# Kernel tuning notes

Measured on AMD Instinct MI355X. Metric: run time of the kernel, lower is better.

Reference implementation:

```python
import jax, jax.numpy as jnp
import numpy as np

WS = 7            # cubic window
HEADS = 6
DIM = 96          # attention channel dim (concat of two half-streams)
CH = 48           # per-stream channels (dim // 2)
HID = 384         # int(dim * mlp_ratio)
N = WS ** 3       # 343 tokens per window
EPS = 1e-5


def _rel_pos_index():
    c = np.stack(np.meshgrid(np.arange(WS), np.arange(WS), np.arange(WS), indexing='ij')).reshape(3, -1)
    rel = (c[:, :, None] - c[:, None, :]).transpose(1, 2, 0) + (WS - 1)
    rel[:, :, 0] *= (2 * WS - 1) * (2 * WS - 1)
    rel[:, :, 1] *= (2 * WS - 1)
    return rel.sum(-1)  # (N, N) int

RPI = jnp.asarray(_rel_pos_index())


def _ln(x, g, b):
    m = x.mean(-1, keepdims=True)
    v = ((x - m) ** 2).mean(-1, keepdims=True)
    return (x - m) * jax.lax.rsqrt(v + EPS) * g + b


def _win_part(x):
    B, H, W, T, C = x.shape
    x = x.reshape(B, H // WS, WS, W // WS, WS, T // WS, WS, C)
    return x.transpose(0, 1, 3, 5, 2, 4, 6, 7).reshape(-1, WS, WS, WS, C)


def _win_rev(w, B, H, W, T):
    C = w.shape[-1]
    x = w.reshape(B, H // WS, W // WS, T // WS, WS, WS, WS, C)
    return x.transpose(0, 1, 4, 2, 5, 3, 6, 7).reshape(B, H, W, T, C)


def _chessboard(wa, wb, gd, gh, gw):
    C = wa.shape[-1]
    a = wa.reshape(gd, gh, gw, WS, WS, WS, C)
    b = wb.reshape(gd, gh, gw, WS, WS, WS, C)
    i = jnp.arange(gd)[:, None, None]
    j = jnp.arange(gh)[None, :, None]
    k = jnp.arange(gw)[None, None, :]
    m = (((i + j + k) % 2) == 0)[..., None, None, None, None]
    return (jnp.where(m, a, b).reshape(-1, WS, WS, WS, C),
            jnp.where(m, b, a).reshape(-1, WS, WS, WS, C))


def _attn(x, mask, rpb, qkv_w, qkv_b, proj_w, proj_b):
    B_, n, C = x.shape
    hd = C // HEADS
    qkv = (x @ qkv_w + qkv_b).reshape(B_, n, 3, HEADS, hd).transpose(2, 0, 3, 1, 4)
    q, k, v = qkv[0] * (hd ** -0.5), qkv[1], qkv[2]
    att = jnp.einsum('bhnd,bhmd->bhnm', q, k)
    att = att + rpb[RPI].transpose(2, 0, 1)[None]   # relative position bias gather
    att = att + mask[:, None]                        # shift mask; B_ == nW since B == 1
    att = jax.nn.softmax(att, axis=-1)
    out = jnp.einsum('bhnm,bhmd->bhnd', att, v).transpose(0, 2, 1, 3).reshape(B_, n, C)
    return out @ proj_w + proj_b


def _mlp(x, w1, b1, w2, b2):
    return jax.nn.gelu(x @ w1 + b1, approximate=False) @ w2 + b2


def _forward(x_a, x_b, mask_matrix, n1a_g, n1a_b, n1b_g, n1b_b,
             rpb_a, qkvw_a, qkvb_a, projw_a, projb_a,
             rpb_b, qkvw_b, qkvb_b, projw_b, projb_b,
             n2a_g, n2a_b, n2b_g, n2b_b,
             fc1w_a, fc1b_a, fc2w_a, fc2b_a, fc1w_b, fc1b_b, fc2w_b, fc2b_b,
             gw1, gw2, gb2, H, W, T):
    B, L, _ = x_a.shape
    sa0, sb0 = x_a, x_b
    a = _ln(x_a, n1a_g, n1a_b).reshape(B, H, W, T, CH)
    b = _ln(x_b, n1b_g, n1b_b).reshape(B, H, W, T, CH)
    # chessboard cross-stream shuffle of windows (shifted-window branch)
    ca, cb = _chessboard(_win_part(a), _win_part(b), H // WS, W // WS, T // WS)
    a_cr = _win_rev(ca, B, H, W, T)
    b_cr = _win_rev(cb, B, H, W, T)
    neg, pos, dims = (-3, -3, -3), (3, 3, 3), (1, 2, 3)
    sa, sb = jnp.roll(a, neg, dims), jnp.roll(b, neg, dims)
    sac, sbc = jnp.roll(a_cr, neg, dims), jnp.roll(b_cr, neg, dims)
    xa_w = _win_part(jnp.concatenate([sa, sbc], -1)).reshape(-1, N, DIM)
    xb_w = _win_part(jnp.concatenate([sb, sac], -1)).reshape(-1, N, DIM)
    oa = _attn(xa_w, mask_matrix, rpb_a, qkvw_a, qkvb_a, projw_a, projb_a)
    ob = _attn(xb_w, mask_matrix, rpb_b, qkvw_b, qkvb_b, projw_b, projb_b)
    oa = jnp.roll(_win_rev(oa.reshape(-1, WS, WS, WS, DIM), B, H, W, T), pos, dims)[..., :CH].reshape(B, L, CH)
    ob = jnp.roll(_win_rev(ob.reshape(-1, WS, WS, WS, DIM), B, H, W, T), pos, dims)[..., :CH].reshape(B, L, CH)
    x_a = sa0 + oa
    x_b = sb0 + ob
    x_a = x_a + _mlp(_ln(x_a, n2a_g, n2a_b), fc1w_a, fc1b_a, fc2w_a, fc2b_a)
    x_b = x_b + _mlp(_ln(x_b, n2b_g, n2b_b), fc1w_b, fc1b_b, fc2w_b, fc2b_b)
    g = jax.nn.sigmoid(jnp.maximum(x_a.mean(1) @ gw1, 0.0) @ gw2 + gb2)[:, :, None]  # (B,1,1)
    x_a = x_a + g * x_b
    return x_a, x_b


def setup_inputs():
    key = jax.random.key(0)
    ks = iter(jax.random.split(key, 24))
    H = W = T = 35
    L = H * W * T
    nW = (H // WS) * (W // WS) * (T // WS)
    p = lambda shape: jax.random.normal(next(ks), shape, jnp.float32) * 0.02
    d = {
        'x_a': jax.random.normal(next(ks), (1, L, CH), jnp.float32),
        'x_b': jax.random.normal(next(ks), (1, L, CH), jnp.float32),
        'mask_matrix': jax.random.normal(next(ks), (nW, N, N), jnp.float32),
        'n1a_g': jnp.ones((CH,), jnp.float32), 'n1a_b': jnp.zeros((CH,), jnp.float32),
        'n1b_g': jnp.ones((CH,), jnp.float32), 'n1b_b': jnp.zeros((CH,), jnp.float32),
        'rpb_a': p(((2 * WS - 1) ** 3, HEADS)),
        'qkvw_a': p((DIM, 3 * DIM)), 'qkvb_a': jnp.zeros((3 * DIM,), jnp.float32),
        'projw_a': p((DIM, DIM)), 'projb_a': jnp.zeros((DIM,), jnp.float32),
        'rpb_b': p(((2 * WS - 1) ** 3, HEADS)),
        'qkvw_b': p((DIM, 3 * DIM)), 'qkvb_b': jnp.zeros((3 * DIM,), jnp.float32),
        'projw_b': p((DIM, DIM)), 'projb_b': jnp.zeros((DIM,), jnp.float32),
        'n2a_g': jnp.ones((CH,), jnp.float32), 'n2a_b': jnp.zeros((CH,), jnp.float32),
        'n2b_g': jnp.ones((CH,), jnp.float32), 'n2b_b': jnp.zeros((CH,), jnp.float32),
        'fc1w_a': p((CH, HID)), 'fc1b_a': jnp.zeros((HID,), jnp.float32),
        'fc2w_a': p((HID, CH)), 'fc2b_a': jnp.zeros((CH,), jnp.float32),
        'fc1w_b': p((CH, HID)), 'fc1b_b': jnp.zeros((HID,), jnp.float32),
        'fc2w_b': p((HID, CH)), 'fc2b_b': jnp.zeros((CH,), jnp.float32),
        'gw1': p((CH, CH // 4)), 'gw2': p((CH // 4, 1)),
        'gb2': jnp.full((1,), -2.0, jnp.float32),
        'H': H, 'W': W, 'T': T,
    }
    return d


def reference(x_a, x_b, mask_matrix, n1a_g, n1a_b, n1b_g, n1b_b,
              rpb_a, qkvw_a, qkvb_a, projw_a, projb_a,
              rpb_b, qkvw_b, qkvb_b, projw_b, projb_b,
              n2a_g, n2a_b, n2b_g, n2b_b,
              fc1w_a, fc1b_a, fc2w_a, fc2b_a, fc1w_b, fc1b_b, fc2w_b, fc2b_b,
              gw1, gw2, gb2, H, W, T):
    return _forward(x_a, x_b, mask_matrix, n1a_g, n1a_b, n1b_g, n1b_b,
                    rpb_a, qkvw_a, qkvb_a, projw_a, projb_a,
                    rpb_b, qkvw_b, qkvb_b, projw_b, projb_b,
                    n2a_g, n2a_b, n2b_g, n2b_b,
                    fc1w_a, fc1b_a, fc2w_a, fc2b_a, fc1w_b, fc1b_b, fc2w_b, fc2b_b,
                    gw1, gw2, gb2, H, W, T)
```

## Files before the change

kernel.cpp:

```cpp
#include <hip/hip_runtime.h>
#include <hip/hip_fp16.h>

#define LQ    42875
#define NTOK  343
#define X1SZ  2058000

#define OFF_MEAN 0
#define OFF_QKV  36928
#define OFF_WF   12500000
#define OFF_RPB  12600000
#define OFF_MASKH 13400000
#define QKV_BYTES_NEEDED 56100000ull
#define MASKH_BYTES_NEEDED 83100000ull

typedef _Float16 f16x8 __attribute__((ext_vector_type(8)));
typedef float f32x4 __attribute__((ext_vector_type(4)));
union B128 { uint4 u; f16x8 h; _Float16 e[8]; };
union U2H { unsigned u; __half2 h; };

__device__ __forceinline__ int src_index(int w, int i, int& par) {
  int gi = w / 25, gj = (w / 5) % 5, gk = w % 5;
  int ph = i / 49, pw = (i / 7) % 7, pt = i % 7;
  int hs = gi * 7 + ph + 3; if (hs >= 35) hs -= 35;
  int wd = gj * 7 + pw + 3; if (wd >= 35) wd -= 35;
  int td = gk * 7 + pt + 3; if (td >= 35) td -= 35;
  par = ((hs / 7) + (wd / 7) + (td / 7)) & 1;
  return (hs * 35 + wd) * 35 + td;
}

__global__ __launch_bounds__(64) void k_init(float* __restrict__ ws) {
  if (threadIdx.x < 49) ws[threadIdx.x] = 0.f;
}

__global__ __launch_bounds__(256) void k_pack(
    const float* __restrict__ w1a, const float* __restrict__ w1b,
    const float* __restrict__ w2a, const float* __restrict__ w2b,
    const float* __restrict__ qwa, const float* __restrict__ qwb,
    float* __restrict__ ws) {
  int idx = blockIdx.x * 256 + threadIdx.x;
  if (idx >= 17664) return;
  uint4* WFB = (uint4*)(ws + OFF_WF);
  unsigned short h[8];
  uint4* dst;
  if (idx < 10752) {
    int s = idx / 5376, r = idx - s * 5376;
    uint4* WF = WFB + (size_t)s * 5376;
    if (r < 3072) {
      int jn = r / 128, t = r - jn * 128, kk = t / 64, lane = t - kk * 64;
      int q = lane >> 4, n = lane & 15;
      const float* w1 = s ? w1b : w1a;
      int j = jn * 16 + n;
#pragma unroll
      for (int e = 0; e < 8; e++) {
        int k = kk * 32 + q * 8 + e;
        float v = (k < 48) ? w1[k * 384 + j] : 0.f;
        h[e] = __half_as_ushort(__float2half(v));
      }
    } else {
      int rr = r - 3072;
      int kt = rr / 192, t = rr - kt * 192, cn = t / 64, lane = t - cn * 64;
      int q = lane >> 4, n = lane & 15;
      const float* w2 = s ? w2b : w2a;
      int c = cn * 16 + n;
#pragma unroll
      for (int e = 0; e < 8; e++) {
        int j = kt * 32 + q * 8 + e;
        h[e] = __half_as_ushort(__float2half(w2[j * 48 + c]));
      }
    }
    dst = WF + r;
  } else {
    int idx2 = idx - 10752;
    int s = idx2 / 3456, r = idx2 - s * 3456;
    int jn = r / 192, t = r - jn * 192, kk = t / 64, lane = t - kk * 64;
    int q = lane >> 4, n = lane & 15;
    const float* qw = s ? qwb : qwa;
    int j = jn * 16 + n;
#pragma unroll
    for (int e = 0; e < 8; e++) {
      int k = kk * 32 + q * 8 + e;
      h[e] = __half_as_ushort(__float2half(qw[k * 288 + j]));
    }
    dst = WFB + 10752 + (size_t)s * 3456 + r;
  }
  uint4 u;
  u.x = (unsigned)h[0] | ((unsigned)h[1] << 16);
  u.y = (unsigned)h[2] | ((unsigned)h[3] << 16);
  u.z = (unsigned)h[4] | ((unsigned)h[5] << 16);
  u.w = (unsigned)h[6] | ((unsigned)h[7] << 16);
  *dst = u;
}

__global__ __launch_bounds__(256) void k_rpb(
    const float* __restrict__ rpa, const float* __restrict__ rpbp,
    float* __restrict__ ws) {
  int sh = blockIdx.y;
  int s = sh / 6, h = sh - s * 6;
  int idx = blockIdx.x * 256 + threadIdx.x;
  if (idx >= 117649) return;
  int ir = idx / 343, j = idx - ir * 343;
  int bi = (ir / 49) * 169 + ((ir / 7) % 7) * 13 + (ir % 7) + 1098;
  int bj = (j / 49) * 169 + ((j / 7) % 7) * 13 + (j % 7);
  const float* rp = s ? rpbp : rpa;
  ((__half*)(ws + OFF_RPB))[(size_t)sh * 117992 + ir * 344 + j] =
      __float2half(rp[(bi - bj) * 6 + h]);
}

__global__ __launch_bounds__(256) void k_maskh(
    const float* __restrict__ mask, __half* __restrict__ mh) {
  int row = blockIdx.x;
  const float* src = mask + (size_t)row * 343;
  __half* dst = mh + (size_t)row * 344;
  for (int c = threadIdx.x; c < 343; c += 256)
    dst[c] = __float2half(src[c]);
  if (threadIdx.x == 0) dst[343] = __float2half(0.f);
}

__global__ __launch_bounds__(256) void k_qkv(
    const float* __restrict__ xa, const float* __restrict__ xb,
    const float* __restrict__ ga, const float* __restrict__ ba,
    const float* __restrict__ gb, const float* __restrict__ bb,
    const float* __restrict__ qba, const float* __restrict__ qbb,
    const float* __restrict__ ws, __half* __restrict__ qkvh) {
  __shared__ uint4 LDSB[2368];
  int s = blockIdx.z;
  int tid = threadIdx.x;
  int wid = tid >> 6, lane = tid & 63;
  int quad = lane >> 4, n15 = lane & 15;
  uint4* WR = LDSB + wid * 592;
  _Float16* th = (_Float16*)WR;
  int tbase = blockIdx.x * 64 + wid * 16;

  if (lane < 32) {
    int tt = lane & 15, which = lane >> 4;
    int t = tbase + tt;
    float v[48];
    bool wr = false, dup = false;
    if (t < LQ) {
      int w = t / 343, i = t - w * 343;
      int par; int src = src_index(w, i, par);
      const float* xr; const float* G; const float* B;
      bool doit;
      if (which == 0) { xr = (s ? xb : xa) + src * 48; G = s ? gb : ga; B = s ? bb : ba; doit = true; dup = (par == 1); }
      else            { xr = (s ? xa : xb) + src * 48; G = s ? ga : gb; B = s ? ba : bb; doit = (par == 0); }
      if (doit) {
        float sm = 0.f, sq = 0.f;
#pragma unroll
        for (int q4 = 0; q4 < 12; q4++) {
          float4 tv = ((const float4*)xr)[q4];
          v[4 * q4] = tv.x; v[4 * q4 + 1] = tv.y; v[4 * q4 + 2] = tv.z; v[4 * q4 + 3] = tv.w;
          sm += tv.x + tv.y + tv.z + tv.w;
          sq += tv.x * tv.x + tv.y * tv.y + tv.z * tv.z + tv.w * tv.w;
        }
        float m = sm * (1.f / 48.f);
        float r = rsqrtf(sq * (1.f / 48.f) - m * m + 1e-5f);
#pragma unroll
        for (int k = 0; k < 48; k++) v[k] = (v[k] - m) * r * G[k] + B[k];
        wr = true;
      }
    } else if (which == 0) {
#pragma unroll
      for (int k = 0; k < 48; k++) v[k] = 0.f;
      wr = true; dup = true;
    }
    if (wr) {
#pragma unroll
      for (int c6 = 0; c6 < 6; c6++) {
        unsigned short h[8];
#pragma unroll
        for (int e = 0; e < 8; e++) h[e] = __half_as_ushort(__float2half(v[c6 * 8 + e]));
        uint4 u;
        u.x = (unsigned)h[0] | ((unsigned)h[1] << 16);
        u.y = (unsigned)h[2] | ((unsigned)h[3] << 16);
        u.z = (unsigned)h[4] | ((unsigned)h[5] << 16);
        u.w = (unsigned)h[6] | ((unsigned)h[7] << 16);
        WR[(which * 6 + c6) * 16 + tt] = u;
        if (dup) WR[(6 + c6) * 16 + tt] = u;
      }
    }
  }

  B128 ax0, ax1, ax2;
  ax0.u = WR[(0 + quad) * 16 + n15];
  ax1.u = WR[(4 + quad) * 16 + n15];
  ax2.u = WR[(8 + quad) * 16 + n15];

  const uint4* QF = (const uint4*)(ws + OFF_WF) + 10752 + (size_t)s * 3456;
  const float* QB = s ? qbb : qba;
  const f32x4 ZC = {0.f, 0.f, 0.f, 0.f};

  for (int jn = 0; jn < 18; jn++) {
    B128 b0, b1, b2;
    b0.u = QF[(jn * 3 + 0) * 64 + lane];
    b1.u = QF[(jn * 3 + 1) * 64 + lane];
    b2.u = QF[(jn * 3 + 2) * 64 + lane];
    f32x4 c = __builtin_amdgcn_mfma_f32_16x16x32_f16(ax0.h, b0.h, ZC, 0, 0, 0);
    c = __builtin_amdgcn_mfma_f32_16x16x32_f16(ax1.h, b1.h, c, 0, 0, 0);
    c = __builtin_amdgcn_mfma_f32_16x16x32_f16(ax2.h, b2.h, c, 0, 0, 0);
    float bias = QB[jn * 16 + n15];
    float scale = (jn < 6) ? 0.25f : 1.0f;
#pragma unroll
    for (int r = 0; r < 4; r++)
      th[(quad * 4 + r) * 296 + jn * 16 + n15] = (_Float16)((c[r] + bias) * scale);
  }
  for (int e = lane; e < 576; e += 64) {
    int row = e / 36, cc = e - row * 36;
    int t = tbase + row;
    if (t < LQ)
      ((uint4*)qkvh)[(size_t)(s * LQ + t) * 36 + cc] = WR[row * 37 + cc];
  }
}

template <bool H16>
__global__ __launch_bounds__(256) void k_attn(
    const __half* __restrict__ rpbmat,
    const void* __restrict__ maskp, __half* __restrict__ qkvh) {
  int bid = blockIdx.x;
  int xcd = bid & 7, q8 = bid >> 3;
  int u = q8 / 12, inst = q8 - u * 12;
  int w = u * 8 + xcd;
  if (w >= 125) return;
  int s = inst & 1, h = inst >> 1;

  __shared__ uint4 FRAG[1664];
  uint4* Kf4 = FRAG;
  uint4* Vf4 = FRAG + 704;
  _Float16* Vfh = (_Float16*)(FRAG + 704);
  _Float16* Pbh = (_Float16*)(FRAG + 1408);

  int tid = threadIdx.x;
  const uint4 Z4 = {0u, 0u, 0u, 0u};
  for (int e = tid; e < 1408; e += 256) FRAG[e] = Z4;
  __syncthreads();

  size_t wbase = (size_t)((s * 125 + w) * NTOK) * 288;
  for (int i = tid; i < NTOK; i += 256) {
    const uint4* row = (const uint4*)(qkvh + wbase + (size_t)i * 288) + (h * 2);
    uint4 k0 = row[12], k1 = row[13];
    B128 v0, v1; v0.u = row[24]; v1.u = row[25];
    int n = i & 15, it = i >> 4;
    Kf4[it * 32 + n] = k0;
    Kf4[it * 32 + 16 + n] = k1;
    int vbase = ((i >> 5) * 64 + ((i >> 3) & 3) * 16) * 8 + (i & 7);
#pragma unroll
    for (int d = 0; d < 8; d++) {
      Vfh[vbase + d * 8] = v0.e[d];
      Vfh[vbase + (d + 8) * 8] = v1.e[d];
    }
  }
  __syncthreads();

  int wid = tid >> 6, lane = tid & 63;
  int quad = lane >> 4, n15 = lane & 15;
  const f32x4 ZC = {0.f, 0.f, 0.f, 0.f};
  __half* obh = qkvh;
  const __half* rbase = rpbmat + (size_t)(s * 6 + h) * 117992;

  _Float16* Pw = Pbh + wid * 512;
  int slotA = quad ^ (n15 & 6);
  int slotB = (4 + quad) ^ (n15 & 6);
  int rslot = (2 * quad) ^ (n15 & 6);
  int ja0 = quad * 4;

  for (int it = wid; it < 22; it += 4) {
    int i0 = it * 16;
    int irow = i0 + n15; if (irow > 342) irow = 342;
    const __half* rrow = rbase + (size_t)irow * 344;
    const __half* mrow = nullptr; const float* mrowf = nullptr;
    if constexpr (H16) mrow = (const __half*)maskp + ((size_t)w * 343 + irow) * 344;
    else mrowf = (const float*)maskp + ((size_t)w * 343 + irow) * 343;

    B128 qbits;
    int qtok = i0 + n15;
    if (quad < 2 && qtok < NTOK)
      qbits.u = *((const uint4*)(qkvh + wbase + (size_t)qtok * 288) + h * 2 + (quad & 1));
    else
      qbits.u = Z4;
    f32x4 acc = ZC;
    float ls = 0.f;

    float bcur[8], bnxt[8];
    auto loadb = [&](int jt, float* b) {
      if constexpr (H16) {
        const __half* mp = mrow + jt * 32 + ja0;
        const __half* rp2 = rrow + jt * 32 + ja0;
        uint2 ma = *(const uint2*)mp;
        uint2 mb = *(const uint2*)(mp + 16);
        uint2 ra = *(const uint2*)rp2;
        uint2 rb = *(const uint2*)(rp2 + 16);
        U2H x0, x1, x2, x3, y0, y1, y2, y3;
        x0.u = ma.x; x1.u = ma.y; x2.u = mb.x; x3.u = mb.y;
        y0.u = ra.x; y1.u = ra.y; y2.u = rb.x; y3.u = rb.y;
        float2 f;
        f = __half22float2(__hadd2(x0.h, y0.h)); b[0] = f.x; b[1] = f.y;
        f = __half22float2(__hadd2(x1.h, y1.h)); b[2] = f.x; b[3] = f.y;
        f = __half22float2(__hadd2(x2.h, y2.h)); b[4] = f.x; b[5] = f.y;
        f = __half22float2(__hadd2(x3.h, y3.h)); b[6] = f.x; b[7] = f.y;
      } else {
        const float* mp = mrowf + jt * 32 + ja0;
        const __half* rp2 = rrow + jt * 32 + ja0;
#pragma unroll
        for (int r = 0; r < 4; r++) {
          b[r] = mp[r] + __half2float(rp2[r]);
          b[4 + r] = mp[16 + r] + __half2float(rp2[16 + r]);
        }
      }
    };
    loadb(0, bcur);

    for (int j32 = 0; j32 < 11; j32++) {
      if (j32 < 10) loadb(j32 + 1, bnxt);
      B128 kb0, kb1;
      kb0.u = Kf4[(j32 * 2) * 32 + ((quad & 1) << 4) + n15];
      kb1.u = Kf4[(j32 * 2 + 1) * 32 + ((quad & 1) << 4) + n15];
      if (quad >= 2) { kb0.u = Z4; kb1.u = Z4; }
      f32x4 s0 = __builtin_amdgcn_mfma_f32_16x16x32_f16(kb0.h, qbits.h, ZC, 0, 0, 0);
      f32x4 s1 = __builtin_amdgcn_mfma_f32_16x16x32_f16(kb1.h, qbits.h, ZC, 0, 0, 0);
      bool last = (j32 == 10);
      float p0[4], p1[4];
#pragma unroll
      for (int r = 0; r < 4; r++) {
        float b1 = bcur[4 + r];
        if (last && (quad * 4 + r) >= 7) b1 = -1e30f;
        p0[r] = __expf(s0[r] + bcur[r]);
        p1[r] = __expf(s1[r] + b1);
        ls += p0[r] + p1[r];
      }
      U2H c0, c1, c2, c3;
      c0.h = __floats2half2_rn(p0[0], p0[1]);
      c1.h = __floats2half2_rn(p0[2], p0[3]);
      c2.h = __floats2half2_rn(p1[0], p1[1]);
      c3.h = __floats2half2_rn(p1[2], p1[3]);
      uint2 w0; w0.x = c0.u; w0.y = c1.u;
      uint2 w1; w1.x = c2.u; w1.y = c3.u;
      *(uint2*)(Pw + n15 * 32 + slotA * 4) = w0;
      *(uint2*)(Pw + n15 * 32 + slotB * 4) = w1;
      B128 pa, vbits;
      pa.u = *(const uint4*)(Pw + n15 * 32 + rslot * 4);
      vbits.u = Vf4[j32 * 64 + lane];
      acc = __builtin_amdgcn_mfma_f32_16x16x32_f16(pa.h, vbits.h, acc, 0, 0, 0);
#pragma unroll
      for (int e = 0; e < 8; e++) bcur[e] = bnxt[e];
    }
    ls += __shfl_xor(ls, 16);
    ls += __shfl_xor(ls, 32);
#pragma unroll
    for (int r = 0; r < 4; r++) {
      float lr = __shfl(ls, quad * 4 + r);
      int ir = i0 + quad * 4 + r;
      if (ir < 343)
        obh[wbase + (size_t)ir * 288 + h * 16 + n15] = __float2half(acc[r] * (1.f / lr));
    }
  }
}

__global__ __launch_bounds__(384) void k_proj(
    const __half* __restrict__ qkvh,
    const float* __restrict__ xa0, const float* __restrict__ xb0,
    const float* __restrict__ pwa, const float* __restrict__ pba,
    const float* __restrict__ pwb, const float* __restrict__ pbb,
    float* __restrict__ out) {
  int sw = blockIdx.x; int s = sw / 125, w = sw - s * 125;
  int i = threadIdx.x;
  if (i >= NTOK) return;
  const float* Wt = s ? pwb : pwa;
  const float* Bi = s ? pbb : pba;
  const uint4* orow = (const uint4*)(qkvh + (size_t)((s * 125 + w) * NTOK + i) * 288);
  float acc[48];
#pragma unroll
  for (int c = 0; c < 48; c++) acc[c] = 0.f;
#pragma unroll
  for (int k8 = 0; k8 < 12; k8++) {
    B128 ov; ov.u = orow[k8];
#pragma unroll
    for (int e = 0; e < 8; e++) {
      float x = (float)ov.e[e];
      const float* wr = Wt + (k8 * 8 + e) * 96;
#pragma unroll
      for (int c = 0; c < 48; c++) acc[c] = fmaf(x, wr[c], acc[c]);
    }
  }
  int par; int src = src_index(w, i, par);
  const float* x0 = (s ? xb0 : xa0) + src * 48;
  float* dst = out + s * X1SZ + src * 48;
#pragma unroll
  for (int q = 0; q < 12; q++) {
    float4 xv = ((const float4*)x0)[q];
    float4 o;
    o.x = xv.x + acc[4 * q + 0] + Bi[4 * q + 0];
    o.y = xv.y + acc[4 * q + 1] + Bi[4 * q + 1];
    o.z = xv.z + acc[4 * q + 2] + Bi[4 * q + 2];
    o.w = xv.w + acc[4 * q + 3] + Bi[4 * q + 3];
    ((float4*)dst)[q] = o;
  }
}

__global__ __launch_bounds__(256) void k_mlp(
    const float* __restrict__ g2a, const float* __restrict__ b2a,
    const float* __restrict__ g2b, const float* __restrict__ b2b,
    const float* __restrict__ fb1a, const float* __restrict__ fb2a,
    const float* __restrict__ fb1b, const float* __restrict__ fb2b,
    float* __restrict__ out, float* __restrict__ ws) {
  __shared__ uint4 Xf[512];
  __shared__ uint4 tbu[320];
  __shared__ float red[48];
  int s = blockIdx.z;
  int tid = threadIdx.x;
  int wid = tid >> 6, lane = tid & 63;
  int quad = lane >> 4, n15 = lane & 15;
  if (tid < 48) red[tid] = 0.f;
  __syncthreads();

  const float* B1 = s ? fb1b : fb1a;
  const float* B2 = s ? fb2b : fb2a;
  const uint4* W1F = (const uint4*)(ws + OFF_WF) + (size_t)s * 5376;
  const uint4* W2F = W1F + 3072;
  int tbase = blockIdx.x * 64 + wid * 16;
  float* outs = out + (size_t)s * X1SZ;

  if (lane < 16) {
    int t = tbase + lane;
    float v[48];
    if (t < LQ) {
      const float* row = outs + (size_t)t * 48;
      float sm = 0.f, sq = 0.f;
#pragma unroll
      for (int q4 = 0; q4 < 12; q4++) {
        float4 tv = ((const float4*)row)[q4];
        v[4 * q4] = tv.x; v[4 * q4 + 1] = tv.y; v[4 * q4 + 2] = tv.z; v[4 * q4 + 3] = tv.w;
        sm += tv.x + tv.y + tv.z + tv.w;
        sq += tv.x * tv.x + tv.y * tv.y + tv.z * tv.z + tv.w * tv.w;
      }
      float m = sm * (1.f / 48.f);
      float r = rsqrtf(sq * (1.f / 48.f) - m * m + 1e-5f);
      const float* G = s ? g2b : g2a;
      const float* B = s ? b2b : b2a;
#pragma unroll
      for (int k = 0; k < 48; k++) v[k] = (v[k] - m) * r * G[k] + B[k];
    } else {
#pragma unroll
      for (int k = 0; k < 48; k++) v[k] = 0.f;
    }
#pragma unroll
    for (int kc = 0; kc < 8; kc++) {
      uint4 u = {0u, 0u, 0u, 0u};
      if (kc < 6) {
        unsigned short h[8];
#pragma unroll
        for (int e = 0; e < 8; e++) h[e] = __half_as_ushort(__float2half(v[kc * 8 + e]));
        u.x = (unsigned)h[0] | ((unsigned)h[1] << 16);
        u.y = (unsigned)h[2] | ((unsigned)h[3] << 16);
        u.z = (unsigned)h[4] | ((unsigned)h[5] << 16);
        u.w = (unsigned)h[6] | ((unsigned)h[7] << 16);
      }
      Xf[wid * 128 + kc * 16 + lane] = u;
    }
  }

  _Float16* mytb = (_Float16*)(tbu + wid * 80);
  const uint4* mytb4 = tbu + wid * 80;
  const f32x4 ZC = {0.f, 0.f, 0.f, 0.f};
  f32x4 oacc[3] = {ZC, ZC, ZC};
  B128 ax0, ax1;
  ax0.u = Xf[wid * 128 + quad * 16 + n15];
  ax1.u = Xf[wid * 128 + (4 + quad) * 16 + n15];

  for (int kt = 0; kt < 12; kt++) {
    int jn0 = kt * 2, jn1 = jn0 + 1;
    B128 w0, w1, w2, w3;
    w0.u = W1F[jn0 * 128 + lane];
    w1.u = W1F[jn0 * 128 + 64 + lane];
    w2.u = W1F[jn1 * 128 + lane];
    w3.u = W1F[jn1 * 128 + 64 + lane];
    f32x4 a0 = __builtin_amdgcn_mfma_f32_16x16x32_f16(ax0.h, w0.h, ZC, 0, 0, 0);
    a0 = __builtin_amdgcn_mfma_f32_16x16x32_f16(ax1.h, w1.h, a0, 0, 0, 0);
    f32x4 a1 = __builtin_amdgcn_mfma_f32_16x16x32_f16(ax0.h, w2.h, ZC, 0, 0, 0);
    a1 = __builtin_amdgcn_mfma_f32_16x16x32_f16(ax1.h, w3.h, a1, 0, 0, 0);
    float bz0 = B1[jn0 * 16 + n15], bz1 = B1[jn1 * 16 + n15];
#pragma unroll
    for (int r = 0; r < 4; r++) {
      float h0 = a0[r] + bz0;
      h0 = 0.5f * h0 * (1.f + erff(h0 * 0.70710678118654752f));
      float h1 = a1[r] + bz1;
      h1 = 0.5f * h1 * (1.f + erff(h1 * 0.70710678118654752f));
      int rowb = (quad * 4 + r) * 40;
      mytb[rowb + n15] = (_Float16)h0;
      mytb[rowb + 16 + n15] = (_Float16)h1;
    }
    B128 pa; pa.u = mytb4[n15 * 5 + quad];
    B128 c0, c1, c2;
    c0.u = W2F[kt * 192 + lane];
    c1.u = W2F[kt * 192 + 64 + lane];
    c2.u = W2F[kt * 192 + 128 + lane];
    oacc[0] = __builtin_amdgcn_mfma_f32_16x16x32_f16(pa.h, c0.h, oacc[0], 0, 0, 0);
    oacc[1] = __builtin_amdgcn_mfma_f32_16x16x32_f16(pa.h, c1.h, oacc[1], 0, 0, 0);
    oacc[2] = __builtin_amdgcn_mfma_f32_16x16x32_f16(pa.h, c2.h, oacc[2], 0, 0, 0);
  }

  float b2v[3];
#pragma unroll
  for (int cn = 0; cn < 3; cn++) b2v[cn] = B2[cn * 16 + n15];
  float gsum[3] = {0.f, 0.f, 0.f};
#pragma unroll
  for (int r = 0; r < 4; r++) {
    int t = tbase + quad * 4 + r;
    bool val = t < LQ;
    float* orow = outs + (size_t)(val ? t : 0) * 48;
#pragma unroll
    for (int cn = 0; cn < 3; cn++) {
      float fin = 0.f;
      if (val) {
        fin = orow[cn * 16 + n15] + oacc[cn][r] + b2v[cn];
        orow[cn * 16 + n15] = fin;
      }
      gsum[cn] += fin;
    }
  }
  if (s == 0) {
#pragma unroll
    for (int cn = 0; cn < 3; cn++) {
      float v = gsum[cn];
      v += __shfl_xor(v, 16); v += __shfl_xor(v, 32);
      if (quad == 0) atomicAdd(&red[cn * 16 + n15], v);
    }
  }
  __syncthreads();
  if (s == 0 && tid < 48) atomicAdd(ws + OFF_MEAN + tid, red[tid]);
}

__global__ __launch_bounds__(64) void k_gate(
    const float* __restrict__ ws_mean, const float* __restrict__ gw1,
    const float* __restrict__ gw2, const float* __restrict__ gb2,
    float* __restrict__ g) {
  int j = threadIdx.x;
  float t = 0.f;
  if (j < 12) {
    for (int c = 0; c < 48; c++)
      t = fmaf(ws_mean[c] * (1.f / (float)LQ), gw1[c * 12 + j], t);
    t = fmaxf(t, 0.f) * gw2[j];
  }
  for (int off = 32; off > 0; off >>= 1) t += __shfl_down(t, off);
  if (j == 0) *g = 1.f / (1.f + __expf(-(t + gb2[0])));
}

__global__ __launch_bounds__(256) void k_gadd(float* __restrict__ out,
                                              const float* __restrict__ g) {
  int i = blockIdx.x * 256 + threadIdx.x;
  if (i >= X1SZ / 4) return;
  float gv = *g;
  float4* a = (float4*)out;
  const float4* b = (const float4*)(out + X1SZ);
  float4 x = a[i], y = b[i];
  x.x = fmaf(gv, y.x, x.x);
  x.y = fmaf(gv, y.y, x.y);
  x.z = fmaf(gv, y.z, x.z);
  x.w = fmaf(gv, y.w, x.w);
  a[i] = x;
}

extern "C" void kernel_launch(void* const* d_in, const int* in_sizes, int n_in,
                              void* d_out, int out_size, void* d_ws, size_t ws_size,
                              hipStream_t stream) {
  const float* xa    = (const float*)d_in[0];
  const float* xb    = (const float*)d_in[1];
  const float* mask  = (const float*)d_in[2];
  const float* n1ag  = (const float*)d_in[3];
  const float* n1ab  = (const float*)d_in[4];
  const float* n1bg  = (const float*)d_in[5];
  const float* n1bb  = (const float*)d_in[6];
  const float* rpba  = (const float*)d_in[7];
  const float* qkvwa = (const float*)d_in[8];
  const float* qkvba = (const float*)d_in[9];
  const float* pwa   = (const float*)d_in[10];
  const float* pba   = (const float*)d_in[11];
  const float* rpbb  = (const float*)d_in[12];
  const float* qkvwb = (const float*)d_in[13];
  const float* qkvbb = (const float*)d_in[14];
  const float* pwb   = (const float*)d_in[15];
  const float* pbb   = (const float*)d_in[16];
  const float* n2ag  = (const float*)d_in[17];
  const float* n2ab  = (const float*)d_in[18];
  const float* n2bg  = (const float*)d_in[19];
  const float* n2bb  = (const float*)d_in[20];
  const float* w1a   = (const float*)d_in[21];
  const float* fb1a  = (const float*)d_in[22];
  const float* w2a   = (const float*)d_in[23];
  const float* fb2a  = (const float*)d_in[24];
  const float* w1b   = (const float*)d_in[25];
  const float* fb1b  = (const float*)d_in[26];
  const float* w2b   = (const float*)d_in[27];
  const float* fb2b  = (const float*)d_in[28];
  const float* gw1   = (const float*)d_in[29];
  const float* gw2   = (const float*)d_in[30];
  const float* gb2   = (const float*)d_in[31];
  float* ws  = (float*)d_ws;
  float* out = (float*)d_out;

  if (ws_size < QKV_BYTES_NEEDED) return;
  __half* qkvh = (__half*)(ws + OFF_QKV);
  bool bigmask = ws_size >= MASKH_BYTES_NEEDED;

  hipLaunchKernelGGL(k_init, dim3(1), dim3(64), 0, stream, ws);
  hipLaunchKernelGGL(k_pack, dim3(69), dim3(256), 0, stream,
                     w1a, w1b, w2a, w2b, qkvwa, qkvwb, ws);
  hipLaunchKernelGGL(k_rpb, dim3(460, 12), dim3(256), 0, stream,
                     rpba, rpbb, ws);
  if (bigmask)
    hipLaunchKernelGGL(k_maskh, dim3(42875), dim3(256), 0, stream,
                       mask, (__half*)(ws + OFF_MASKH));
  hipLaunchKernelGGL(k_qkv, dim3(670, 1, 2), dim3(256), 0, stream,
                     xa, xb, n1ag, n1ab, n1bg, n1bb,
                     qkvba, qkvbb, ws, qkvh);
  if (bigmask)
    hipLaunchKernelGGL((k_attn<true>), dim3(1536), dim3(256), 0, stream,
                       (const __half*)(ws + OFF_RPB),
                       (const void*)(ws + OFF_MASKH), qkvh);
  else
    hipLaunchKernelGGL((k_attn<false>), dim3(1536), dim3(256), 0, stream,
                       (const __half*)(ws + OFF_RPB), (const void*)mask, qkvh);
  hipLaunchKernelGGL(k_proj, dim3(250), dim3(384), 0, stream,
                     qkvh, xa, xb, pwa, pba, pwb, pbb, out);
  hipLaunchKernelGGL(k_mlp, dim3(670, 1, 2), dim3(256), 0, stream,
                     n2ag, n2ab, n2bg, n2bb,
                     fb1a, fb2a, fb1b, fb2b, out, ws);
  hipLaunchKernelGGL(k_gate, dim3(1), dim3(64), 0, stream,
                     ws + OFF_MEAN, gw1, gw2, gb2, ws + OFF_MEAN + 48);
  hipLaunchKernelGGL(k_gadd, dim3(2011), dim3(256), 0, stream,
                     out, ws + OFF_MEAN + 48);
}
```

Measured before the change: 449.1 us.

## Feed softmax probabilities to PV MFMA from registers, fuse small kernels

Reorders the V fragment layout in LDS so that the attention probabilities computed by each lane can be passed straight from registers as the A operand of the PV MFMA. This removes the per-tile LDS write, read and transpose of P and shrinks shared memory. The gate computation is folded into the gated-add kernel, each block recomputing the scalar gate, and the accumulator zeroing is merged into the pack kernel, which removes two launches. The mask fp16 conversion is vectorised to four elements per thread.

```diff
diff --git a/kernel.cpp b/kernel.cpp
--- a/kernel.cpp
+++ b/kernel.cpp
@@ -28,15 +28,12 @@
   return (hs * 35 + wd) * 35 + td;
 }
 
-__global__ __launch_bounds__(64) void k_init(float* __restrict__ ws) {
-  if (threadIdx.x < 49) ws[threadIdx.x] = 0.f;
-}
-
 __global__ __launch_bounds__(256) void k_pack(
     const float* __restrict__ w1a, const float* __restrict__ w1b,
     const float* __restrict__ w2a, const float* __restrict__ w2b,
     const float* __restrict__ qwa, const float* __restrict__ qwb,
     float* __restrict__ ws) {
+  if (blockIdx.x == 0 && threadIdx.x < 49) ws[OFF_MEAN + threadIdx.x] = 0.f;
   int idx = blockIdx.x * 256 + threadIdx.x;
   if (idx >= 17664) return;
   uint4* WFB = (uint4*)(ws + OFF_WF);
@@ -108,12 +105,19 @@
 
 __global__ __launch_bounds__(256) void k_maskh(
     const float* __restrict__ mask, __half* __restrict__ mh) {
-  int row = blockIdx.x;
-  const float* src = mask + (size_t)row * 343;
-  __half* dst = mh + (size_t)row * 344;
-  for (int c = threadIdx.x; c < 343; c += 256)
-    dst[c] = __float2half(src[c]);
-  if (threadIdx.x == 0) dst[343] = __float2half(0.f);
+  int idx = blockIdx.x * 256 + threadIdx.x;
+  if (idx >= 42875 * 86) return;
+  int row = idx / 86, c = (idx - row * 86) * 4;
+  const float* src = mask + (size_t)row * 343 + c;
+  float v0 = src[0];
+  float v1 = (c + 1 < 343) ? src[1] : 0.f;
+  float v2 = (c + 2 < 343) ? src[2] : 0.f;
+  float v3 = (c + 3 < 343) ? src[3] : 0.f;
+  U2H a, b;
+  a.h = __floats2half2_rn(v0, v1);
+  b.h = __floats2half2_rn(v2, v3);
+  uint2 o; o.x = a.u; o.y = b.u;
+  *(uint2*)(mh + (size_t)row * 344 + c) = o;
 }
 
 __global__ __launch_bounds__(256) void k_qkv(
@@ -222,11 +226,10 @@
   if (w >= 125) return;
   int s = inst & 1, h = inst >> 1;
 
-  __shared__ uint4 FRAG[1664];
+  __shared__ uint4 FRAG[1408];
   uint4* Kf4 = FRAG;
   uint4* Vf4 = FRAG + 704;
   _Float16* Vfh = (_Float16*)(FRAG + 704);
-  _Float16* Pbh = (_Float16*)(FRAG + 1408);
 
   int tid = threadIdx.x;
   const uint4 Z4 = {0u, 0u, 0u, 0u};
@@ -241,11 +244,15 @@
     int n = i & 15, it = i >> 4;
     Kf4[it * 32 + n] = k0;
     Kf4[it * 32 + 16 + n] = k1;
-    int vbase = ((i >> 5) * 64 + ((i >> 3) & 3) * 16) * 8 + (i & 7);
+    int il = i & 31, t5 = i >> 5;
+    int qq, ee;
+    if (il < 16) { qq = il >> 2; ee = il & 3; }
+    else { qq = (il - 16) >> 2; ee = 4 + ((il - 16) & 3); }
+    int vb = (t5 * 64 + qq * 16) * 8 + ee;
 #pragma unroll
     for (int d = 0; d < 8; d++) {
-      Vfh[vbase + d * 8] = v0.e[d];
-      Vfh[vbase + (d + 8) * 8] = v1.e[d];
+      Vfh[vb + d * 8] = v0.e[d];
+      Vfh[vb + (d + 8) * 8] = v1.e[d];
     }
   }
   __syncthreads();
@@ -255,11 +262,6 @@
   const f32x4 ZC = {0.f, 0.f, 0.f, 0.f};
   __half* obh = qkvh;
   const __half* rbase = rpbmat + (size_t)(s * 6 + h) * 117992;
-
-  _Float16* Pw = Pbh + wid * 512;
-  int slotA = quad ^ (n15 & 6);
-  int slotB = (4 + quad) ^ (n15 & 6);
-  int rslot = (2 * quad) ^ (n15 & 6);
   int ja0 = quad * 4;
 
   for (int it = wid; it < 22; it += 4) {
@@ -331,13 +333,9 @@
       c1.h = __floats2half2_rn(p0[2], p0[3]);
       c2.h = __floats2half2_rn(p1[0], p1[1]);
       c3.h = __floats2half2_rn(p1[2], p1[3]);
-      uint2 w0; w0.x = c0.u; w0.y = c1.u;
-      uint2 w1; w1.x = c2.u; w1.y = c3.u;
-      *(uint2*)(Pw + n15 * 32 + slotA * 4) = w0;
-      *(uint2*)(Pw + n15 * 32 + slotB * 4) = w1;
-      B128 pa, vbits;
-      pa.u = *(const uint4*)(Pw + n15 * 32 + rslot * 4);
-      vbits.u = Vf4[j32 * 64 + lane];
+      B128 pa;
+      pa.u.x = c0.u; pa.u.y = c1.u; pa.u.z = c2.u; pa.u.w = c3.u;
+      B128 vbits; vbits.u = Vf4[j32 * 64 + lane];
       acc = __builtin_amdgcn_mfma_f32_16x16x32_f16(pa.h, vbits.h, acc, 0, 0, 0);
 #pragma unroll
       for (int e = 0; e < 8; e++) bcur[e] = bnxt[e];
@@ -528,26 +526,26 @@
   if (s == 0 && tid < 48) atomicAdd(ws + OFF_MEAN + tid, red[tid]);
 }
 
-__global__ __launch_bounds__(64) void k_gate(
-    const float* __restrict__ ws_mean, const float* __restrict__ gw1,
-    const float* __restrict__ gw2, const float* __restrict__ gb2,
-    float* __restrict__ g) {
-  int j = threadIdx.x;
-  float t = 0.f;
-  if (j < 12) {
-    for (int c = 0; c < 48; c++)
-      t = fmaf(ws_mean[c] * (1.f / (float)LQ), gw1[c * 12 + j], t);
-    t = fmaxf(t, 0.f) * gw2[j];
-  }
-  for (int off = 32; off > 0; off >>= 1) t += __shfl_down(t, off);
-  if (j == 0) *g = 1.f / (1.f + __expf(-(t + gb2[0])));
-}
-
-__global__ __launch_bounds__(256) void k_gadd(float* __restrict__ out,
-                                              const float* __restrict__ g) {
-  int i = blockIdx.x * 256 + threadIdx.x;
+__global__ __launch_bounds__(256) void k_gadd(
+    float* __restrict__ out, const float* __restrict__ ws_mean,
+    const float* __restrict__ gw1, const float* __restrict__ gw2,
+    const float* __restrict__ gb2) {
+  __shared__ float gs;
+  int tid = threadIdx.x;
+  if (tid < 64) {
+    float t = 0.f;
+    if (tid < 12) {
+      for (int c = 0; c < 48; c++)
+        t = fmaf(ws_mean[c] * (1.f / (float)LQ), gw1[c * 12 + tid], t);
+      t = fmaxf(t, 0.f) * gw2[tid];
+    }
+    for (int off = 32; off > 0; off >>= 1) t += __shfl_down(t, off);
+    if (tid == 0) gs = 1.f / (1.f + __expf(-(t + gb2[0])));
+  }
+  __syncthreads();
+  float gv = gs;
+  int i = blockIdx.x * 256 + tid;
   if (i >= X1SZ / 4) return;
-  float gv = *g;
   float4* a = (float4*)out;
   const float4* b = (const float4*)(out + X1SZ);
   float4 x = a[i], y = b[i];
@@ -600,13 +598,12 @@
   __half* qkvh = (__half*)(ws + OFF_QKV);
   bool bigmask = ws_size >= MASKH_BYTES_NEEDED;
 
-  hipLaunchKernelGGL(k_init, dim3(1), dim3(64), 0, stream, ws);
   hipLaunchKernelGGL(k_pack, dim3(69), dim3(256), 0, stream,
                      w1a, w1b, w2a, w2b, qkvwa, qkvwb, ws);
   hipLaunchKernelGGL(k_rpb, dim3(460, 12), dim3(256), 0, stream,
                      rpba, rpbb, ws);
   if (bigmask)
-    hipLaunchKernelGGL(k_maskh, dim3(42875), dim3(256), 0, stream,
+    hipLaunchKernelGGL(k_maskh, dim3(14405), dim3(256), 0, stream,
                        mask, (__half*)(ws + OFF_MASKH));
   hipLaunchKernelGGL(k_qkv, dim3(670, 1, 2), dim3(256), 0, stream,
                      xa, xb, n1ag, n1ab, n1bg, n1bb,
@@ -623,8 +620,6 @@
   hipLaunchKernelGGL(k_mlp, dim3(670, 1, 2), dim3(256), 0, stream,
                      n2ag, n2ab, n2bg, n2bb,
                      fb1a, fb2a, fb1b, fb2b, out, ws);
-  hipLaunchKernelGGL(k_gate, dim3(1), dim3(64), 0, stream,
-                     ws + OFF_MEAN, gw1, gw2, gb2, ws + OFF_MEAN + 48);
   hipLaunchKernelGGL(k_gadd, dim3(2011), dim3(256), 0, stream,
-                     out, ws + OFF_MEAN + 48);
-}
+                     out, ws + OFF_MEAN, gw1, gw2, gb2);
+}
```

After: 423.8 us. 1.06x faster.
